# Performance work log

Hardware: AMD Instinct MI355X
Metric: run time of the kernel (lower is better)

The kernel has to match this reference:

```python
import jax, jax.numpy as jnp
import numpy as np

LOCATE_KERNEL_STD = 0.2
MEANS = jnp.array([0.0, 0.2, 0.4, 0.6, 0.8, 1.0], dtype=jnp.float32)  # setof6


def setup_inputs() -> dict:
    key = jax.random.key(0)
    k1, k2 = jax.random.split(key)
    weights = jax.random.uniform(k1, (6,), dtype=jnp.float32)
    inp = jax.random.normal(k2, (4096, 8194), dtype=jnp.float32)
    return {"weights": weights, "inp": inp}


def reference(weights, inp):
    B, L = inp.shape
    ln = L - 2
    pos = jnp.arange(ln, dtype=jnp.float32) / ln          # pos * 1.0 / ln
    std = jnp.float32(LOCATE_KERNEL_STD)
    # Normal.log_prob(pos).exp() -> Gaussian pdf, [6, ln]
    z = (pos[None, :] - MEANS[:, None]) / std
    pdf = jnp.exp(-0.5 * z * z) / (std * jnp.sqrt(2.0 * jnp.pi))
    row = weights @ pdf                                   # [ln]
    return jnp.broadcast_to(row[None, :], (B, ln))
```

## Files before the change

kernel.cpp:

```cpp
#include <hip/hip_runtime.h>

#define LN 8192
#define B_ROWS 4096
#define NMEANS 6

__global__ void __launch_bounds__(256)
row_kernel(const float* __restrict__ w, float* __restrict__ row) {
    int j = blockIdx.x * blockDim.x + threadIdx.x;
    if (j >= LN) return;
    const float inv_std = 5.0f;
    const float norm    = 1.9947114020071633897f;
    float pos = (float)j * (1.0f / (float)LN);
    float acc = 0.0f;
#pragma unroll
    for (int k = 0; k < NMEANS; ++k) {
        float m = 0.2f * (float)k;
        float z = (pos - m) * inv_std;
        acc += w[k] * expf(-0.5f * z * z);
    }
    row[j] = acc * norm;
}

__global__ void __launch_bounds__(256)
bcast_kernel(const float4* __restrict__ row4, float4* __restrict__ out4,
             long long n4) {
    long long i      = (long long)blockIdx.x * blockDim.x + threadIdx.x;
    long long stride = (long long)gridDim.x * blockDim.x;
    const int mask = LN / 4 - 1;
    for (; i < n4; i += stride) {
        out4[i] = row4[(int)i & mask];
    }
}

extern "C" void kernel_launch(void* const* d_in, const int* in_sizes, int n_in,
                              void* d_out, int out_size, void* d_ws, size_t ws_size,
                              hipStream_t stream) {
    const float* w = (const float*)d_in[0];
    float* out = (float*)d_out;
    float* row = (float*)d_ws;

    row_kernel<<<dim3(LN / 256), dim3(256), 0, stream>>>(w, row);

    long long n4 = (long long)out_size / 4;
    bcast_kernel<<<dim3(2048), dim3(256), 0, stream>>>(
        (const float4*)row, (float4*)out, n4);
}
```

Measured before the change: 31.44 us.

## Fuse row computation into broadcast kernel with per-block recompute and nontemporal stores

```diff
diff --git a/kernel.cpp b/kernel.cpp
--- a/kernel.cpp
+++ b/kernel.cpp
@@ -4,31 +4,45 @@
 #define B_ROWS 4096
 #define NMEANS 6
 
+#define COLS_PER_BLOCK 1024
+#define ROWS_PER_BLOCK 16
+#define COL_SEGS (LN / COLS_PER_BLOCK)
+#define ROW_CHUNKS (B_ROWS / ROWS_PER_BLOCK)
+
+typedef float v4f __attribute__((ext_vector_type(4)));
+
 __global__ void __launch_bounds__(256)
-row_kernel(const float* __restrict__ w, float* __restrict__ row) {
-    int j = blockIdx.x * blockDim.x + threadIdx.x;
-    if (j >= LN) return;
+fused_kernel(const float* __restrict__ w, float* __restrict__ out) {
+    const int bid     = blockIdx.x;
+    const int colSeg  = bid & (COL_SEGS - 1);
+    const int rowBase = (bid >> 3) * ROWS_PER_BLOCK;
+
+    const int j0 = colSeg * COLS_PER_BLOCK + threadIdx.x * 4;
+
+    float wk[NMEANS];
+#pragma unroll
+    for (int k = 0; k < NMEANS; ++k) wk[k] = w[k];
+
     const float inv_std = 5.0f;
     const float norm    = 1.9947114020071633897f;
-    float pos = (float)j * (1.0f / (float)LN);
-    float acc = 0.0f;
+
+    v4f v;
 #pragma unroll
-    for (int k = 0; k < NMEANS; ++k) {
-        float m = 0.2f * (float)k;
-        float z = (pos - m) * inv_std;
-        acc += w[k] * expf(-0.5f * z * z);
+    for (int e = 0; e < 4; ++e) {
+        float pos = (float)(j0 + e) * (1.0f / (float)LN);
+        float acc = 0.0f;
+#pragma unroll
+        for (int k = 0; k < NMEANS; ++k) {
+            float z = (pos - 0.2f * (float)k) * inv_std;
+            acc += wk[k] * expf(-0.5f * z * z);
+        }
+        v[e] = acc * norm;
     }
-    row[j] = acc * norm;
-}
 
-__global__ void __launch_bounds__(256)
-bcast_kernel(const float4* __restrict__ row4, float4* __restrict__ out4,
-             long long n4) {
-    long long i      = (long long)blockIdx.x * blockDim.x + threadIdx.x;
-    long long stride = (long long)gridDim.x * blockDim.x;
-    const int mask = LN / 4 - 1;
-    for (; i < n4; i += stride) {
-        out4[i] = row4[(int)i & mask];
+    float* base = out + (long long)rowBase * LN + j0;
+#pragma unroll
+    for (int r = 0; r < ROWS_PER_BLOCK; ++r) {
+        __builtin_nontemporal_store(v, (v4f*)(base + (long long)r * LN));
     }
 }
 
@@ -37,11 +51,6 @@
                               hipStream_t stream) {
     const float* w = (const float*)d_in[0];
     float* out = (float*)d_out;
-    float* row = (float*)d_ws;
 
-    row_kernel<<<dim3(LN / 256), dim3(256), 0, stream>>>(w, row);
-
-    long long n4 = (long long)out_size / 4;
-    bcast_kernel<<<dim3(2048), dim3(256), 0, stream>>>(
-        (const float4*)row, (float4*)out, n4);
+    fused_kernel<<<dim3(COL_SEGS * ROW_CHUNKS), dim3(256), 0, stream>>>(w, out);
 }
```

After: 28.35 us. 1.11x faster.
